# Performance work log

Measured on AMD Instinct MI355X. Metric: run time of the kernel, lower is better.

Reference implementation:

```python
import jax, jax.numpy as jnp
import numpy as np

INDIM = 128
OUTDIM = 256
GRID = 16


def setup_inputs() -> dict:
    key = jax.random.key(0)
    kx, kc = jax.random.split(key)
    x = jax.random.normal(kx, (32768, INDIM), dtype=jnp.float32)
    # fouriercoeffs: (2, outdim, indim, gridsize), init randn / (sqrt(indim)*sqrt(gridsize))
    fouriercoeffs = jax.random.normal(kc, (2, OUTDIM, INDIM, GRID), dtype=jnp.float32) / (
        np.sqrt(INDIM) * np.sqrt(GRID)
    )
    bias = jnp.zeros((1, OUTDIM), dtype=jnp.float32)
    return {"x": x, "fouriercoeffs": fouriercoeffs, "bias": bias}


def reference(x, fouriercoeffs, bias):
    orig_shape = x.shape
    x2 = x.reshape(-1, INDIM)  # (N, indim)
    k = jnp.arange(1, GRID + 1, dtype=x2.dtype)  # (gridsize,)
    x_scaled = x2[:, :, None] * k  # (N, indim, gridsize)
    y = (
        jnp.einsum("nig,oig->no", jnp.cos(x_scaled), fouriercoeffs[0])
        + jnp.einsum("nig,oig->no", jnp.sin(x_scaled), fouriercoeffs[1])
        + bias
    )
    return y.reshape(*orig_shape[:-1], OUTDIM)
```

## Files before the change

kernel.cpp:

```cpp
#include <hip/hip_runtime.h>
#include <cstdint>

#define IN_DIM   128
#define OUT_DIM  256
#define NROWS    32768
#define BM       64
#define NSTEPS   16
#define STR      65

typedef unsigned short u16;
typedef __attribute__((ext_vector_type(8))) __bf16 bf16x8;
typedef __attribute__((ext_vector_type(4))) float  f32x4;

__global__ __launch_bounds__(256) void kan_prep(const float* __restrict__ C,
                                                u16* __restrict__ Bpack) {
    const int o = threadIdx.x;
    const int i = blockIdx.x;
    const int t = blockIdx.y;
    const float* src = C + (((size_t)(t * OUT_DIM + o) * IN_DIM + i) * 16);
    bf16x8 lo = {}, hi = {};
#pragma unroll
    for (int g = 0; g < 8; ++g) {
        lo[g] = (__bf16)src[g];
        hi[g] = (__bf16)src[8 + g];
    }
    const int ko = i * 4 + t * 2;
    bf16x8* dst = (bf16x8*)Bpack;
    dst[(size_t)ko * OUT_DIM + o]       = lo;
    dst[(size_t)(ko + 1) * OUT_DIM + o] = hi;
}

__global__ __launch_bounds__(512, 4) void kan_gemm(const float* __restrict__ x,
                                                   const u16* __restrict__ Bpack,
                                                   const float* __restrict__ bias,
                                                   float* __restrict__ out) {
    __shared__ __align__(16) u16 Asm[2][32 * STR * 8];

    const int tid  = threadIdx.x;
    const int lane = tid & 63;
    const int wid  = tid >> 6;
    const int lrow = lane & 15;
    const int lk   = lane >> 4;
    const int wm   = wid & 1;
    const int wn   = wid >> 1;
    const int m0   = blockIdx.x * BM;

    const int tr  = tid >> 3;
    const int til = tid & 7;

    const f32x4 vzero = {0.f, 0.f, 0.f, 0.f};
    f32x4 acc[2][4];
#pragma unroll
    for (int a = 0; a < 2; ++a)
#pragma unroll
        for (int b = 0; b < 4; ++b) acc[a][b] = vzero;

    const bf16x8* Bv = (const bf16x8*)Bpack;
    bf16x8* Av0 = (bf16x8*)Asm[0];
    bf16x8* Av1 = (bf16x8*)Asm[1];

    const float* xrow = x + (size_t)(m0 + tr) * IN_DIM + til;
    const int bcol = wn * 64 + lrow;

    auto gen = [&](bf16x8* Av, float xv) {
        float s1, c1;
        __sincosf(xv, &s1, &c1);
        const float t2 = 2.f * c1;
        bf16x8 qc0 = {}, qc1 = {}, qs0 = {}, qs1 = {};
        float cp = c1, sp = s1;
        float cc = t2 * c1 - 1.f, sc = t2 * s1;
        qc0[0] = (__bf16)cp;  qs0[0] = (__bf16)sp;
        qc0[1] = (__bf16)cc;  qs0[1] = (__bf16)sc;
#pragma unroll
        for (int g = 3; g <= 16; ++g) {
            const float cn = t2 * cc - cp;
            const float sn = t2 * sc - sp;
            cp = cc; sp = sc; cc = cn; sc = sn;
            const int idx = g - 1;
            if (idx < 8) { qc0[idx] = (__bf16)cc;      qs0[idx] = (__bf16)sc; }
            else         { qc1[idx - 8] = (__bf16)cc;  qs1[idx - 8] = (__bf16)sc; }
        }
        const int kob = til * 4;
        Av[(kob + 0) * STR + tr] = qc0;
        Av[(kob + 1) * STR + tr] = qc1;
        Av[(kob + 2) * STR + tr] = qs0;
        Av[(kob + 3) * STR + tr] = qs1;
    };

    bf16x8 bg[4];
#pragma unroll
    for (int f = 0; f < 4; ++f)
        bg[f] = Bv[(size_t)lk * OUT_DIM + bcol + f * 16];

    float xn = xrow[8];
    gen(Av0, xrow[0]);
    __syncthreads();

    for (int kt = 0; kt < NSTEPS; ++kt) {
        bf16x8* Avc = (kt & 1) ? Av1 : Av0;
        bf16x8* Avn = (kt & 1) ? Av0 : Av1;

        if (kt + 1 < NSTEPS) {
            gen(Avn, xn);
            xn = xrow[((kt + 2) & (NSTEPS - 1)) * 8];
        }

#pragma unroll
        for (int ks = 0; ks < 8; ++ks) {
            const int ktn = (ks == 7) ? ((kt + 1) & (NSTEPS - 1)) : kt;
            const int ksn = (ks + 1) & 7;
            const size_t kqn = (size_t)(ktn * 32 + ksn * 4 + lk);
            bf16x8 bgn[4];
#pragma unroll
            for (int f = 0; f < 4; ++f)
                bgn[f] = Bv[kqn * OUT_DIM + bcol + f * 16];

            const int kq = ks * 4 + lk;
            bf16x8 af[2];
#pragma unroll
            for (int f = 0; f < 2; ++f)
                af[f] = Avc[kq * STR + wm * 32 + f * 16 + lrow];
#pragma unroll
            for (int fm = 0; fm < 2; ++fm)
#pragma unroll
                for (int fn = 0; fn < 4; ++fn)
                    acc[fm][fn] = __builtin_amdgcn_mfma_f32_16x16x32_bf16(
                        af[fm], bg[fn], acc[fm][fn], 0, 0, 0);
#pragma unroll
            for (int f = 0; f < 4; ++f) bg[f] = bgn[f];
        }
        __syncthreads();
    }

#pragma unroll
    for (int fn = 0; fn < 4; ++fn) {
        const int col = wn * 64 + fn * 16 + lrow;
        const float bv = bias[col];
#pragma unroll
        for (int fm = 0; fm < 2; ++fm) {
            const int r0 = m0 + wm * 32 + fm * 16 + lk * 4;
            float* op = out + (size_t)r0 * OUT_DIM + col;
#pragma unroll
            for (int j = 0; j < 4; ++j)
                op[(size_t)j * OUT_DIM] = acc[fm][fn][j] + bv;
        }
    }
}

extern "C" void kernel_launch(void* const* d_in, const int* in_sizes, int n_in,
                              void* d_out, int out_size, void* d_ws, size_t ws_size,
                              hipStream_t stream) {
    const float* x    = (const float*)d_in[0];
    const float* fc   = (const float*)d_in[1];
    const float* bias = (const float*)d_in[2];
    float* out        = (float*)d_out;
    u16* Bpack        = (u16*)d_ws;

    kan_prep<<<dim3(IN_DIM, 2), OUT_DIM, 0, stream>>>(fc, Bpack);
    kan_gemm<<<dim3(NROWS / BM), 512, 0, stream>>>(x, Bpack, bias, out);
}
```

Baseline: 88.29 us.

## Switch GEMM to 32x32x16 MFMA with 4-wave blocks and whole-stage B prefetch

Replaces the 16x16x32 bf16 MFMA tiling (8 waves, 2x4 fragments) with 32x32x16 MFMA on 4 waves, each covering all 64 rows and 64 columns. The K loop becomes 32 smaller stages with 4 threads per row generating the Fourier features. All B fragments for the next stage are prefetched into registers in one batch. The aim is fewer LDS A reads per FLOP and better MFMA efficiency. In exchange it uses more registers (16-wide accumulators plus double-buffered B), lowers occupancy (launch bounds 256,2), and has more barrier-separated stages.

```diff
diff --git a/kernel.cpp b/kernel.cpp
--- a/kernel.cpp
+++ b/kernel.cpp
@@ -5,12 +5,12 @@
 #define OUT_DIM  256
 #define NROWS    32768
 #define BM       64
-#define NSTEPS   16
+#define NSTEPS   32
 #define STR      65
 
 typedef unsigned short u16;
-typedef __attribute__((ext_vector_type(8))) __bf16 bf16x8;
-typedef __attribute__((ext_vector_type(4))) float  f32x4;
+typedef __attribute__((ext_vector_type(8)))  __bf16 bf16x8;
+typedef __attribute__((ext_vector_type(16))) float  f32x16;
 
 __global__ __launch_bounds__(256) void kan_prep(const float* __restrict__ C,
                                                 u16* __restrict__ Bpack) {
@@ -30,37 +30,33 @@
     dst[(size_t)(ko + 1) * OUT_DIM + o] = hi;
 }
 
-__global__ __launch_bounds__(512, 4) void kan_gemm(const float* __restrict__ x,
+__global__ __launch_bounds__(256, 2) void kan_gemm(const float* __restrict__ x,
                                                    const u16* __restrict__ Bpack,
                                                    const float* __restrict__ bias,
                                                    float* __restrict__ out) {
-    __shared__ __align__(16) u16 Asm[2][32 * STR * 8];
+    __shared__ __align__(16) u16 Asm[2][16 * STR * 8];
 
     const int tid  = threadIdx.x;
     const int lane = tid & 63;
-    const int wid  = tid >> 6;
-    const int lrow = lane & 15;
-    const int lk   = lane >> 4;
-    const int wm   = wid & 1;
-    const int wn   = wid >> 1;
+    const int wn   = tid >> 6;
+    const int la31 = lane & 31;
+    const int gh   = lane >> 5;
     const int m0   = blockIdx.x * BM;
 
-    const int tr  = tid >> 3;
-    const int til = tid & 7;
+    const int tr  = tid >> 2;
+    const int til = tid & 3;
 
-    const f32x4 vzero = {0.f, 0.f, 0.f, 0.f};
-    f32x4 acc[2][4];
+    f32x16 vz;
 #pragma unroll
-    for (int a = 0; a < 2; ++a)
-#pragma unroll
-        for (int b = 0; b < 4; ++b) acc[a][b] = vzero;
+    for (int r = 0; r < 16; ++r) vz[r] = 0.f;
+    f32x16 acc[2][2] = {{vz, vz}, {vz, vz}};
 
     const bf16x8* Bv = (const bf16x8*)Bpack;
     bf16x8* Av0 = (bf16x8*)Asm[0];
     bf16x8* Av1 = (bf16x8*)Asm[1];
 
     const float* xrow = x + (size_t)(m0 + tr) * IN_DIM + til;
-    const int bcol = wn * 64 + lrow;
+    const int bcol = wn * 64 + la31;
 
     auto gen = [&](bf16x8* Av, float xv) {
         float s1, c1;
@@ -87,12 +83,15 @@
         Av[(kob + 3) * STR + tr] = qs1;
     };
 
-    bf16x8 bg[4];
+    bf16x8 Bcur[8][2], Bnxt[8][2];
+
 #pragma unroll
-    for (int f = 0; f < 4; ++f)
-        bg[f] = Bv[(size_t)lk * OUT_DIM + bcol + f * 16];
-
-    float xn = xrow[8];
+    for (int kw = 0; kw < 8; ++kw)
+#pragma unroll
+        for (int fn = 0; fn < 2; ++fn)
+            Bcur[kw][fn] = Bv[(size_t)((kw >> 1) * 4 + (kw & 1) * 2 + gh) * OUT_DIM
+                              + bcol + fn * 32];
+    float xn = xrow[4];
     gen(Av0, xrow[0]);
     __syncthreads();
 
@@ -100,49 +99,53 @@
         bf16x8* Avc = (kt & 1) ? Av1 : Av0;
         bf16x8* Avn = (kt & 1) ? Av0 : Av1;
 
+        const int ktn = (kt + 1) & (NSTEPS - 1);
+#pragma unroll
+        for (int kw = 0; kw < 8; ++kw)
+#pragma unroll
+            for (int fn = 0; fn < 2; ++fn)
+                Bnxt[kw][fn] = Bv[(size_t)(ktn * 16 + (kw >> 1) * 4 + (kw & 1) * 2 + gh)
+                                  * OUT_DIM + bcol + fn * 32];
+
         if (kt + 1 < NSTEPS) {
             gen(Avn, xn);
-            xn = xrow[((kt + 2) & (NSTEPS - 1)) * 8];
+            xn = xrow[((kt + 2) & (NSTEPS - 1)) * 4];
         }
 
 #pragma unroll
-        for (int ks = 0; ks < 8; ++ks) {
-            const int ktn = (ks == 7) ? ((kt + 1) & (NSTEPS - 1)) : kt;
-            const int ksn = (ks + 1) & 7;
-            const size_t kqn = (size_t)(ktn * 32 + ksn * 4 + lk);
-            bf16x8 bgn[4];
-#pragma unroll
-            for (int f = 0; f < 4; ++f)
-                bgn[f] = Bv[kqn * OUT_DIM + bcol + f * 16];
-
-            const int kq = ks * 4 + lk;
+        for (int kw = 0; kw < 8; ++kw) {
+            const int koL = (kw >> 1) * 4 + (kw & 1) * 2 + gh;
             bf16x8 af[2];
 #pragma unroll
-            for (int f = 0; f < 2; ++f)
-                af[f] = Avc[kq * STR + wm * 32 + f * 16 + lrow];
+            for (int fm = 0; fm < 2; ++fm)
+                af[fm] = Avc[koL * STR + fm * 32 + la31];
 #pragma unroll
             for (int fm = 0; fm < 2; ++fm)
 #pragma unroll
-                for (int fn = 0; fn < 4; ++fn)
-                    acc[fm][fn] = __builtin_amdgcn_mfma_f32_16x16x32_bf16(
-                        af[fm], bg[fn], acc[fm][fn], 0, 0, 0);
+                for (int fn = 0; fn < 2; ++fn)
+                    acc[fm][fn] = __builtin_amdgcn_mfma_f32_32x32x16_bf16(
+                        af[fm], Bcur[kw][fn], acc[fm][fn], 0, 0, 0);
+        }
 #pragma unroll
-            for (int f = 0; f < 4; ++f) bg[f] = bgn[f];
-        }
+        for (int kw = 0; kw < 8; ++kw)
+#pragma unroll
+            for (int fn = 0; fn < 2; ++fn)
+                Bcur[kw][fn] = Bnxt[kw][fn];
         __syncthreads();
     }
 
 #pragma unroll
-    for (int fn = 0; fn < 4; ++fn) {
-        const int col = wn * 64 + fn * 16 + lrow;
+    for (int fn = 0; fn < 2; ++fn) {
+        const int col = bcol + fn * 32;
         const float bv = bias[col];
 #pragma unroll
         for (int fm = 0; fm < 2; ++fm) {
-            const int r0 = m0 + wm * 32 + fm * 16 + lk * 4;
-            float* op = out + (size_t)r0 * OUT_DIM + col;
+            const int rbase = m0 + fm * 32 + 4 * gh;
 #pragma unroll
-            for (int j = 0; j < 4; ++j)
-                op[(size_t)j * OUT_DIM] = acc[fm][fn][j] + bv;
+            for (int r = 0; r < 16; ++r) {
+                const int row = rbase + (r & 3) + 8 * (r >> 2);
+                out[(size_t)row * OUT_DIM + col] = acc[fm][fn][r] + bv;
+            }
         }
     }
 }
@@ -157,5 +160,5 @@
     u16* Bpack        = (u16*)d_ws;
 
     kan_prep<<<dim3(IN_DIM, 2), OUT_DIM, 0, stream>>>(fc, Bpack);
-    kan_gemm<<<dim3(NROWS / BM), 512, 0, stream>>>(x, Bpack, bias, out);
+    kan_gemm<<<dim3(NROWS / BM), 256, 0, stream>>>(x, Bpack, bias, out);
 }
```

After: 79.42 us. 10.0% less time.
